# Optimization experiments

Measured on AMD Instinct MI355X. Metric: run time of the kernel, lower is better.

The kernel has to match this reference:

```python
import jax, jax.numpy as jnp
import numpy as np

MACRO_CURVE_ORDER = 3
MAX_ACTION_LEN = 24
NUM_CURVES = 8
VOCAB = 361
NUM_LAYERS = 6
HID = 32


def setup_inputs() -> dict:
    key = jax.random.key(0)
    ks = iter(jax.random.split(key, 32))
    B, N_PART, P, CTX = 4096, 100, 64, 64

    def lin(k, din, dout):
        k1, k2 = jax.random.split(k)
        s = 1.0 / np.sqrt(din)
        return (jax.random.uniform(k1, (din, dout), jnp.float32, -s, s),
                jax.random.uniform(k2, (dout,), jnp.float32, -s, s))

    fc1_w, fc1_b = lin(next(ks), P, 256)
    fc2_w, fc2_b = lin(next(ks), 256, 256)
    fc3_w, fc3_b = lin(next(ks), CTX + 256, 512)
    fc4_w, fc4_b = lin(next(ks), 512, 256)
    fc5_w, fc5_b = lin(next(ks), 256, 128)
    fc6_w, fc6_b = lin(next(ks), 128, 32)
    fc10_w, fc10_b = lin(next(ks), HID, VOCAB)

    s = 1.0 / np.sqrt(HID)
    lstm_wih = jax.random.uniform(next(ks), (NUM_LAYERS, HID, 4 * HID), jnp.float32, -s, s)
    lstm_whh = jax.random.uniform(next(ks), (NUM_LAYERS, HID, 4 * HID), jnp.float32, -s, s)
    lstm_bih = jax.random.uniform(next(ks), (NUM_LAYERS, 4 * HID), jnp.float32, -s, s)
    lstm_bhh = jax.random.uniform(next(ks), (NUM_LAYERS, 4 * HID), jnp.float32, -s, s)

    return {
        "c": jax.random.normal(next(ks), (B, CTX), jnp.float32),
        "x": jax.random.normal(next(ks), (B, N_PART * P), jnp.float32),
        "hidden": jnp.zeros((NUM_LAYERS, B, HID), jnp.float32),
        "cell": jnp.zeros((NUM_LAYERS, B, HID), jnp.float32),
        "fc1_w": fc1_w, "fc1_b": fc1_b, "fc2_w": fc2_w, "fc2_b": fc2_b,
        "fc3_w": fc3_w, "fc3_b": fc3_b, "fc4_w": fc4_w, "fc4_b": fc4_b,
        "fc5_w": fc5_w, "fc5_b": fc5_b, "fc6_w": fc6_w, "fc6_b": fc6_b,
        "lstm_wih": lstm_wih, "lstm_whh": lstm_whh,
        "lstm_bih": lstm_bih, "lstm_bhh": lstm_bhh,
        "fc10_w": fc10_w, "fc10_b": fc10_b,
        "particle_size": P,
    }


def _lstm_stack(x, h, c, wih, whh, bih, bhh):
    """One time step through 6 stacked LSTM layers (PyTorch cell math)."""
    hs, cs = [], []
    inp = x
    for l in range(NUM_LAYERS):
        gates = inp @ wih[l] + bih[l] + h[l] @ whh[l] + bhh[l]  # (B, 4*HID)
        i, f, g, o = jnp.split(gates, 4, axis=-1)
        i, f, o = jax.nn.sigmoid(i), jax.nn.sigmoid(f), jax.nn.sigmoid(o)
        g = jnp.tanh(g)
        c_new = f * c[l] + i * g
        h_new = o * jnp.tanh(c_new)
        hs.append(h_new)
        cs.append(c_new)
        inp = h_new
    return inp, jnp.stack(hs), jnp.stack(cs)


def reference(c, x, hidden, cell, fc1_w, fc1_b, fc2_w, fc2_b, fc3_w, fc3_b,
              fc4_w, fc4_b, fc5_w, fc5_b, fc6_w, fc6_b,
              lstm_wih, lstm_whh, lstm_bih, lstm_bhh, fc10_w, fc10_b,
              particle_size):
    B = x.shape[0]
    # Belief (particle) encoder with mean pooling.
    xp = x.reshape(B, -1, particle_size)
    xp = jax.nn.relu(xp @ fc1_w + fc1_b)
    xp = jax.nn.relu(xp @ fc2_w + fc2_b)
    xp = xp.mean(axis=-2)  # (B, 256)
    z = jnp.concatenate([c, xp], axis=-1)
    z = jax.nn.relu(z @ fc3_w + fc3_b)
    z = jax.nn.relu(z @ fc4_w + fc4_b)
    z = jax.nn.relu(z @ fc5_w + fc5_b)
    z = jax.nn.relu(z @ fc6_w + fc6_b)  # (B, 32)

    def step(carry, _):
        xt, h, cst = carry
        xt, h, cst = _lstm_stack(xt, h, cst, lstm_wih, lstm_whh, lstm_bih, lstm_bhh)
        logits = xt @ fc10_w + fc10_b  # (B, VOCAB)
        idx = jax.lax.top_k(logits, NUM_CURVES)[1]  # (B, NUM_CURVES)
        return (xt, h, cst), idx

    (_, _, _), idxs = jax.lax.scan(step, (z, hidden, cell), None, length=MAX_ACTION_LEN)
    # (T, B, K) -> (B, T*K)
    preds = jnp.transpose(idxs, (1, 0, 2)).reshape(B, MAX_ACTION_LEN * NUM_CURVES)
    return preds
```

## Files before the change

kernel.cpp:

```cpp
#include <hip/hip_runtime.h>
#include <math.h>

#define BATCH 4096
#define NPART 100
#define PSZ   64

__device__ __forceinline__ void fma4(float4& d, const float s, const float4 v) {
    d.x = fmaf(s, v.x, d.x); d.y = fmaf(s, v.y, d.y);
    d.z = fmaf(s, v.z, d.z); d.w = fmaf(s, v.w, d.w);
}
__device__ __forceinline__ float4 addrelu4(const float4 a, const float4 b) {
    return make_float4(fmaxf(a.x + b.x, 0.f), fmaxf(a.y + b.y, 0.f),
                       fmaxf(a.z + b.z, 0.f), fmaxf(a.w + b.w, 0.f));
}

typedef const __attribute__((address_space(1))) unsigned int  gu32;
typedef __attribute__((address_space(3)))       unsigned int  lu32;
__device__ __forceinline__ void gload_lds16(const float* g, float* l) {
    __builtin_amdgcn_global_load_lds((gu32*)g, (lu32*)l, 16, 0, 0);
}

__device__ __forceinline__ void stage_panel16(const float* __restrict__ w,
                                              float* dst, const int p,
                                              const int wv, const int lane) {
    const float* g = w + p * 4096 + wv * 256 + lane * 4;
    float*       l = dst + wv * 256;
    #pragma unroll
    for (int s = 0; s < 4; ++s)
        gload_lds16(g + s * 1024, l + s * 1024);
}

template<int NRR>
__device__ __forceinline__ void enc_chunk(
    const float* __restrict__ xb, const int rbase,
    const float* __restrict__ w1c, const float* __restrict__ w2,
    float* __restrict__ h1s, float* __restrict__ wpan,
    const int wv, const int lane, const int rg, const int col0,
    const float4 b1a, const float4 b1b, const float4 b2a, const float4 b2b,
    float* msum)
{
    stage_panel16(w2, wpan, 0, wv, lane);

    int rowr[NRR];
    #pragma unroll
    for (int rr = 0; rr < NRR; ++rr)
        rowr[rr] = rbase + ((NRR == 1 && rg >= 4) ? 0 : (rg + 8 * rr));

    float4 a0[NRR], a1[NRR];
    #pragma unroll
    for (int rr = 0; rr < NRR; ++rr) {
        a0[rr] = make_float4(0.f, 0.f, 0.f, 0.f);
        a1[rr] = make_float4(0.f, 0.f, 0.f, 0.f);
    }
    #pragma unroll 2
    for (int k0 = 0; k0 < 64; k0 += 4) {
        float4 bva[4], bvb[4];
        #pragma unroll
        for (int kk = 0; kk < 4; ++kk) {
            bva[kk] = *(const float4*)(w1c + (k0 + kk) * 256);
            bvb[kk] = *(const float4*)(w1c + (k0 + kk) * 256 + 4);
        }
        #pragma unroll
        for (int rr = 0; rr < NRR; ++rr) {
            const float4 av = *(const float4*)(xb + (size_t)rowr[rr] * 64 + k0);
            fma4(a0[rr], av.x, bva[0]); fma4(a0[rr], av.y, bva[1]);
            fma4(a0[rr], av.z, bva[2]); fma4(a0[rr], av.w, bva[3]);
            fma4(a1[rr], av.x, bvb[0]); fma4(a1[rr], av.y, bvb[1]);
            fma4(a1[rr], av.z, bvb[2]); fma4(a1[rr], av.w, bvb[3]);
        }
    }
    #pragma unroll
    for (int rr = 0; rr < NRR; ++rr) {
        const int r = rg + 8 * rr;
        *(float4*)&h1s[r * 260 + col0]     = addrelu4(a0[rr], b1a);
        *(float4*)&h1s[r * 260 + col0 + 4] = addrelu4(a1[rr], b1b);
    }
    __syncthreads();

    float4 c0[NRR], c1[NRR];
    #pragma unroll
    for (int rr = 0; rr < NRR; ++rr) {
        c0[rr] = make_float4(0.f, 0.f, 0.f, 0.f);
        c1[rr] = make_float4(0.f, 0.f, 0.f, 0.f);
    }
    #pragma unroll 1
    for (int p = 0; p < 16; ++p) {
        if (p < 15)
            stage_panel16(w2, wpan + ((p + 1) & 1) * 4096, p + 1, wv, lane);
        const float* wp = wpan + (p & 1) * 4096;
        #pragma unroll
        for (int it = 0; it < 4; ++it) {
            const int kk0 = it * 4;
            float4 bva[4], bvb[4];
            #pragma unroll
            for (int kk = 0; kk < 4; ++kk) {
                bva[kk] = *(const float4*)&wp[(kk0 + kk) * 256 + col0];
                bvb[kk] = *(const float4*)&wp[(kk0 + kk) * 256 + col0 + 4];
            }
            const int kg = p * 16 + kk0;
            #pragma unroll
            for (int rr = 0; rr < NRR; ++rr) {
                const float4 av = *(const float4*)&h1s[(rg + 8 * rr) * 260 + kg];
                fma4(c0[rr], av.x, bva[0]); fma4(c0[rr], av.y, bva[1]);
                fma4(c0[rr], av.z, bva[2]); fma4(c0[rr], av.w, bva[3]);
                fma4(c1[rr], av.x, bvb[0]); fma4(c1[rr], av.y, bvb[1]);
                fma4(c1[rr], av.z, bvb[2]); fma4(c1[rr], av.w, bvb[3]);
            }
        }
        __syncthreads();
    }

    #pragma unroll
    for (int rr = 0; rr < NRR; ++rr) {
        if (NRR == 4 || rg < 4) {
            msum[0] += fmaxf(c0[rr].x + b2a.x, 0.f);
            msum[1] += fmaxf(c0[rr].y + b2a.y, 0.f);
            msum[2] += fmaxf(c0[rr].z + b2a.z, 0.f);
            msum[3] += fmaxf(c0[rr].w + b2a.w, 0.f);
            msum[4] += fmaxf(c1[rr].x + b2b.x, 0.f);
            msum[5] += fmaxf(c1[rr].y + b2b.y, 0.f);
            msum[6] += fmaxf(c1[rr].z + b2b.z, 0.f);
            msum[7] += fmaxf(c1[rr].w + b2b.w, 0.f);
        }
    }
}

__global__ __launch_bounds__(256) void k_encoder(
    const float* __restrict__ x,
    const float* __restrict__ w1, const float* __restrict__ b1,
    const float* __restrict__ w2, const float* __restrict__ b2,
    float* __restrict__ xp)
{
    __shared__ __align__(16) float h1s[32 * 260];
    __shared__ __align__(16) float wpan[2 * 16 * 256];
    const int tid  = threadIdx.x;
    const int b    = blockIdx.x;
    const int lane = tid & 63;
    const int wv   = tid >> 6;
    const int cgw  = lane & 7;
    const int rg   = lane >> 3;
    const int col0 = wv * 64 + cgw * 8;

    const float* xb  = x + (size_t)b * (NPART * PSZ);
    const float* w1c = w1 + col0;
    const float4 b1a = *(const float4*)&b1[col0];
    const float4 b1b = *(const float4*)&b1[col0 + 4];
    const float4 b2a = *(const float4*)&b2[col0];
    const float4 b2b = *(const float4*)&b2[col0 + 4];

    float msum[8] = {0.f,0.f,0.f,0.f,0.f,0.f,0.f,0.f};

    enc_chunk<4>(xb,  0, w1c, w2, h1s, wpan, wv, lane, rg, col0, b1a, b1b, b2a, b2b, msum);
    enc_chunk<4>(xb, 32, w1c, w2, h1s, wpan, wv, lane, rg, col0, b1a, b1b, b2a, b2b, msum);
    enc_chunk<4>(xb, 64, w1c, w2, h1s, wpan, wv, lane, rg, col0, b1a, b1b, b2a, b2b, msum);
    enc_chunk<1>(xb, 96, w1c, w2, h1s, wpan, wv, lane, rg, col0, b1a, b1b, b2a, b2b, msum);

    #pragma unroll
    for (int q = 0; q < 8; ++q) {
        msum[q] += __shfl_xor(msum[q], 8, 64);
        msum[q] += __shfl_xor(msum[q], 16, 64);
        msum[q] += __shfl_xor(msum[q], 32, 64);
    }
    if (rg == 0) {
        float4 o0 = make_float4(msum[0] / 100.f, msum[1] / 100.f,
                                msum[2] / 100.f, msum[3] / 100.f);
        float4 o1 = make_float4(msum[4] / 100.f, msum[5] / 100.f,
                                msum[6] / 100.f, msum[7] / 100.f);
        *(float4*)&xp[(size_t)b * 256 + col0]     = o0;
        *(float4*)&xp[(size_t)b * 256 + col0 + 4] = o1;
    }
}

__global__ __launch_bounds__(256) void k_mlpstm(
    const float* __restrict__ cin, const float* __restrict__ xp,
    const float* __restrict__ w3, const float* __restrict__ b3,
    const float* __restrict__ w4, const float* __restrict__ b4,
    const float* __restrict__ w5, const float* __restrict__ b5,
    const float* __restrict__ w6, const float* __restrict__ b6,
    const float* __restrict__ hid0, const float* __restrict__ cel0,
    const float* __restrict__ wih, const float* __restrict__ whh,
    const float* __restrict__ bih, const float* __restrict__ bhh,
    const float* __restrict__ w10, const float* __restrict__ b10,
    int* __restrict__ out)
{
    __shared__ __align__(16) float smem[15432];
    float (*in0)[320]    = (float(*)[320])(smem);
    float (*h3)[512]     = (float(*)[512])(smem + 2560);
    float (*h4)[256]     = (float(*)[256])(smem + 6656);
    float (*h5)[128]     = (float(*)[128])(smem + 8704);
    float (*xs)[32]      = (float(*)[32])(smem);
    float (*hs)[8][32]   = (float(*)[8][32])(smem + 256);
    float (*cs)[8][32]   = (float(*)[8][32])(smem + 1792);
    float (*gates)[128]  = (float(*)[128])(smem + 3328);
    float (*logits)[361] = (float(*)[361])(smem + 4352);
    float* wldsI         = smem + 7240;
    float* wldsH         = smem + 11336;

    const int tid  = threadIdx.x;
    const int row0 = blockIdx.x * 8;
    const int lane = tid & 63, wv = tid >> 6;

    for (int i = tid; i < 8 * 16; i += 256) {
        int r = i >> 4, q = i & 15;
        *(float4*)&in0[r][q * 4] = *(const float4*)&cin[(size_t)(row0 + r) * 64 + q * 4];
    }
    for (int i = tid; i < 8 * 64; i += 256) {
        int r = i >> 6, q = i & 63;
        *(float4*)&in0[r][64 + q * 4] = *(const float4*)&xp[(size_t)(row0 + r) * 256 + q * 4];
    }
    __syncthreads();

    {
        float a0[8], a1[8];
        #pragma unroll
        for (int r = 0; r < 8; ++r) { a0[r] = 0.f; a1[r] = 0.f; }
        const int c0 = tid, c1 = tid + 256;
        for (int kq = 0; kq < 80; ++kq) {
            const int k0 = kq * 4;
            float wa0 = w3[(k0+0)*512 + c0], wa1 = w3[(k0+1)*512 + c0];
            float wa2 = w3[(k0+2)*512 + c0], wa3 = w3[(k0+3)*512 + c0];
            float wb0 = w3[(k0+0)*512 + c1], wb1 = w3[(k0+1)*512 + c1];
            float wb2 = w3[(k0+2)*512 + c1], wb3 = w3[(k0+3)*512 + c1];
            #pragma unroll
            for (int r = 0; r < 8; ++r) {
                const float4 a = *(const float4*)&in0[r][k0];
                a0[r] = fmaf(a.x, wa0, fmaf(a.y, wa1, fmaf(a.z, wa2, fmaf(a.w, wa3, a0[r]))));
                a1[r] = fmaf(a.x, wb0, fmaf(a.y, wb1, fmaf(a.z, wb2, fmaf(a.w, wb3, a1[r]))));
            }
        }
        const float bb0 = b3[c0], bb1 = b3[c1];
        #pragma unroll
        for (int r = 0; r < 8; ++r) {
            h3[r][c0] = fmaxf(a0[r] + bb0, 0.f);
            h3[r][c1] = fmaxf(a1[r] + bb1, 0.f);
        }
    }
    __syncthreads();

    {
        float ac[8];
        #pragma unroll
        for (int r = 0; r < 8; ++r) ac[r] = 0.f;
        for (int kq = 0; kq < 128; ++kq) {
            const int k0 = kq * 4;
            float w0 = w4[(k0+0)*256 + tid], w1v = w4[(k0+1)*256 + tid];
            float w2v = w4[(k0+2)*256 + tid], w3v = w4[(k0+3)*256 + tid];
            #pragma unroll
            for (int r = 0; r < 8; ++r) {
                const float4 a = *(const float4*)&h3[r][k0];
                ac[r] = fmaf(a.x, w0, fmaf(a.y, w1v, fmaf(a.z, w2v, fmaf(a.w, w3v, ac[r]))));
            }
        }
        const float bb = b4[tid];
        #pragma unroll
        for (int r = 0; r < 8; ++r) h4[r][tid] = fmaxf(ac[r] + bb, 0.f);
    }
    __syncthreads();

    {
        const int c5 = tid & 127, half = tid >> 7;
        float ac[4];
        #pragma unroll
        for (int r = 0; r < 4; ++r) ac[r] = 0.f;
        for (int kq = 0; kq < 64; ++kq) {
            const int k0 = kq * 4;
            float w0 = w5[(k0+0)*128 + c5], w1v = w5[(k0+1)*128 + c5];
            float w2v = w5[(k0+2)*128 + c5], w3v = w5[(k0+3)*128 + c5];
            #pragma unroll
            for (int r = 0; r < 4; ++r) {
                const float4 a = *(const float4*)&h4[half * 4 + r][k0];
                ac[r] = fmaf(a.x, w0, fmaf(a.y, w1v, fmaf(a.z, w2v, fmaf(a.w, w3v, ac[r]))));
            }
        }
        const float bb = b5[c5];
        #pragma unroll
        for (int r = 0; r < 4; ++r) h5[half * 4 + r][c5] = fmaxf(ac[r] + bb, 0.f);
    }
    __syncthreads();

    {
        const int c6 = tid & 31, r = tid >> 5;
        float ac = 0.f;
        for (int kq = 0; kq < 32; ++kq) {
            const int k0 = kq * 4;
            float w0 = w6[(k0+0)*32 + c6], w1v = w6[(k0+1)*32 + c6];
            float w2v = w6[(k0+2)*32 + c6], w3v = w6[(k0+3)*32 + c6];
            const float4 a = *(const float4*)&h5[r][k0];
            ac = fmaf(a.x, w0, fmaf(a.y, w1v, fmaf(a.z, w2v, fmaf(a.w, w3v, ac))));
        }
        xs[r][c6] = fmaxf(ac + b6[c6], 0.f);
    }
    __syncthreads();

    stage_panel16(wih, wldsI, 0, wv, lane);
    stage_panel16(whh, wldsH, 0, wv, lane);

    for (int i = tid; i < 6 * 8 * 32; i += 256) {
        int l = i >> 8, rj = i & 255;
        (&hs[0][0][0])[i] = hid0[(size_t)l * BATCH * 32 + (size_t)row0 * 32 + rj];
        (&cs[0][0][0])[i] = cel0[(size_t)l * BATCH * 32 + (size_t)row0 * 32 + rj];
    }
    __syncthreads();

    const int g  = tid & 127, rg = tid >> 7;
    const int jc = tid & 31,  jr = tid >> 5;

    for (int t = 0; t < 24; ++t) {
        for (int l = 0; l < 6; ++l) {
            const float* inp = (l == 0) ? ((t == 0) ? &xs[0][0] : &hs[5][0][0])
                                        : &hs[l - 1][0][0];
            const float bsum = bih[l * 128 + g] + bhh[l * 128 + g];
            float acc[4] = {bsum, bsum, bsum, bsum};
            #pragma unroll
            for (int k = 0; k < 32; k += 4) {
                float wi0 = wldsI[(k+0)*128 + g], wi1 = wldsI[(k+1)*128 + g];
                float wi2 = wldsI[(k+2)*128 + g], wi3 = wldsI[(k+3)*128 + g];
                float wh0 = wldsH[(k+0)*128 + g], wh1 = wldsH[(k+1)*128 + g];
                float wh2 = wldsH[(k+2)*128 + g], wh3 = wldsH[(k+3)*128 + g];
                #pragma unroll
                for (int rr = 0; rr < 4; ++rr) {
                    const int r = rg * 4 + rr;
                    const float4 ai = *(const float4*)&inp[r * 32 + k];
                    const float4 ah = *(const float4*)&hs[l][r][k];
                    acc[rr] = fmaf(ai.x, wi0, acc[rr]); acc[rr] = fmaf(ai.y, wi1, acc[rr]);
                    acc[rr] = fmaf(ai.z, wi2, acc[rr]); acc[rr] = fmaf(ai.w, wi3, acc[rr]);
                    acc[rr] = fmaf(ah.x, wh0, acc[rr]); acc[rr] = fmaf(ah.y, wh1, acc[rr]);
                    acc[rr] = fmaf(ah.z, wh2, acc[rr]); acc[rr] = fmaf(ah.w, wh3, acc[rr]);
                }
            }
            #pragma unroll
            for (int rr = 0; rr < 4; ++rr) gates[rg * 4 + rr][g] = acc[rr];
            __syncthreads();

            {
                const int ln = (l + 1) % 6;
                stage_panel16(wih, wldsI, ln, wv, lane);
                stage_panel16(whh, wldsH, ln, wv, lane);
            }

            {
                const float gi = gates[jr][jc],      gf = gates[jr][32 + jc];
                const float gg = gates[jr][64 + jc], go = gates[jr][96 + jc];
                const float i_ = 1.f / (1.f + expf(-gi));
                const float f_ = 1.f / (1.f + expf(-gf));
                const float o_ = 1.f / (1.f + expf(-go));
                const float g_ = tanhf(gg);
                const float cn = f_ * cs[l][jr][jc] + i_ * g_;
                cs[l][jr][jc] = cn;
                hs[l][jr][jc] = o_ * tanhf(cn);
            }
            __syncthreads();
        }

        #pragma unroll
        for (int pass = 0; pass < 2; ++pass) {
            const int v = tid + pass * 256;
            if (v < 361) {
                const float bb = b10[v];
                float a8[8];
                #pragma unroll
                for (int r = 0; r < 8; ++r) a8[r] = bb;
                #pragma unroll
                for (int k = 0; k < 32; k += 4) {
                    float w0 = w10[(k+0)*361 + v], w1v = w10[(k+1)*361 + v];
                    float w2v = w10[(k+2)*361 + v], w3v = w10[(k+3)*361 + v];
                    #pragma unroll
                    for (int r = 0; r < 8; ++r) {
                        const float4 a = *(const float4*)&hs[5][r][k];
                        a8[r] = fmaf(a.x, w0, fmaf(a.y, w1v, fmaf(a.z, w2v, fmaf(a.w, w3v, a8[r]))));
                    }
                }
                #pragma unroll
                for (int r = 0; r < 8; ++r) logits[r][v] = a8[r];
            }
        }
        __syncthreads();

        for (int rr = 0; rr < 2; ++rr) {
            const int r = wv * 2 + rr;
            float val[6];
            #pragma unroll
            for (int s = 0; s < 6; ++s) {
                const int v = lane + 64 * s;
                val[s] = (v < 361) ? logits[r][v] : -3.4e38f;
            }
            unsigned msk = 0x3Fu;
            const int rowg = row0 + r;
            for (int sel = 0; sel < 8; ++sel) {
                float bv = -3.4e38f; int bi = 0x7FFFFFFF;
                #pragma unroll
                for (int s = 0; s < 6; ++s) {
                    if (msk & (1u << s)) {
                        const float v2 = val[s]; const int i2 = lane + 64 * s;
                        if (v2 > bv || (v2 == bv && i2 < bi)) { bv = v2; bi = i2; }
                    }
                }
                #pragma unroll
                for (int off = 32; off >= 1; off >>= 1) {
                    const float ov = __shfl_xor(bv, off, 64);
                    const int   oi = __shfl_xor(bi, off, 64);
                    if (ov > bv || (ov == bv && oi < bi)) { bv = ov; bi = oi; }
                }
                if ((bi & 63) == lane) msk &= ~(1u << (bi >> 6));
                if (lane == 0) out[(size_t)rowg * 192 + t * 8 + sel] = bi;
            }
        }
        __syncthreads();
    }
}

extern "C" void kernel_launch(void* const* d_in, const int* in_sizes, int n_in,
                              void* d_out, int out_size, void* d_ws, size_t ws_size,
                              hipStream_t stream) {
    const float* cin  = (const float*)d_in[0];
    const float* x    = (const float*)d_in[1];
    const float* hid0 = (const float*)d_in[2];
    const float* cel0 = (const float*)d_in[3];
    const float* w1 = (const float*)d_in[4];  const float* b1 = (const float*)d_in[5];
    const float* w2 = (const float*)d_in[6];  const float* b2 = (const float*)d_in[7];
    const float* w3 = (const float*)d_in[8];  const float* b3 = (const float*)d_in[9];
    const float* w4 = (const float*)d_in[10]; const float* b4 = (const float*)d_in[11];
    const float* w5 = (const float*)d_in[12]; const float* b5 = (const float*)d_in[13];
    const float* w6 = (const float*)d_in[14]; const float* b6 = (const float*)d_in[15];
    const float* wih = (const float*)d_in[16]; const float* whh = (const float*)d_in[17];
    const float* bih = (const float*)d_in[18]; const float* bhh = (const float*)d_in[19];
    const float* w10 = (const float*)d_in[20]; const float* b10 = (const float*)d_in[21];

    float* xp  = (float*)d_ws;
    int*   out = (int*)d_out;

    k_encoder<<<BATCH, 256, 0, stream>>>(x, w1, b1, w2, b2, xp);
    k_mlpstm<<<BATCH / 8, 256, 0, stream>>>(cin, xp, w3, b3, w4, b4, w5, b5, w6, b6,
                                            hid0, cel0, wih, whh, bih, bhh, w10, b10, out);
}
```

Measured before the change: 2.141 ms.

## Fuse fc10 logits into per-wave top-k registers with transposed fc10 weights

A small pre-kernel transposes fc10_w so each vocab entry's 32 weights are contiguous. In the LSTM kernel, each wave now computes logits only for the two rows it later ranks, keeping them in registers instead of writing them to a shared-memory logits buffer. This drops two block-wide barriers per time step and shrinks shared memory. The cost is less weight reuse: each weight is now read by four waves, and there is an extra kernel launch.

```diff
diff --git a/kernel.cpp b/kernel.cpp
--- a/kernel.cpp
+++ b/kernel.cpp
@@ -28,6 +28,16 @@
     #pragma unroll
     for (int s = 0; s < 4; ++s)
         gload_lds16(g + s * 1024, l + s * 1024);
+}
+
+__global__ __launch_bounds__(256) void k_tw10(
+    const float* __restrict__ w10, float* __restrict__ w10t)
+{
+    const int i = blockIdx.x * 256 + threadIdx.x;
+    if (i < 361 * 32) {
+        const int v = i >> 5, k = i & 31;
+        w10t[i] = w10[k * 361 + v];
+    }
 }
 
 template<int NRR>
@@ -180,21 +190,20 @@
     const float* __restrict__ hid0, const float* __restrict__ cel0,
     const float* __restrict__ wih, const float* __restrict__ whh,
     const float* __restrict__ bih, const float* __restrict__ bhh,
-    const float* __restrict__ w10, const float* __restrict__ b10,
+    const float* __restrict__ w10t, const float* __restrict__ b10,
     int* __restrict__ out)
 {
-    __shared__ __align__(16) float smem[15432];
-    float (*in0)[320]    = (float(*)[320])(smem);
-    float (*h3)[512]     = (float(*)[512])(smem + 2560);
-    float (*h4)[256]     = (float(*)[256])(smem + 6656);
-    float (*h5)[128]     = (float(*)[128])(smem + 8704);
-    float (*xs)[32]      = (float(*)[32])(smem);
-    float (*hs)[8][32]   = (float(*)[8][32])(smem + 256);
-    float (*cs)[8][32]   = (float(*)[8][32])(smem + 1792);
-    float (*gates)[128]  = (float(*)[128])(smem + 3328);
-    float (*logits)[361] = (float(*)[361])(smem + 4352);
-    float* wldsI         = smem + 7240;
-    float* wldsH         = smem + 11336;
+    __shared__ __align__(16) float smem[12544];
+    float (*in0)[320]   = (float(*)[320])(smem);
+    float (*h3)[512]    = (float(*)[512])(smem + 2560);
+    float (*h4)[256]    = (float(*)[256])(smem + 6656);
+    float (*h5)[128]    = (float(*)[128])(smem + 8704);
+    float (*xs)[32]     = (float(*)[32])(smem);
+    float (*hs)[8][32]  = (float(*)[8][32])(smem + 256);
+    float (*cs)[8][32]  = (float(*)[8][32])(smem + 1792);
+    float (*gates)[128] = (float(*)[128])(smem + 3328);
+    float* wldsI        = smem + 4352;
+    float* wldsH        = smem + 8448;
 
     const int tid  = threadIdx.x;
     const int row0 = blockIdx.x * 8;
@@ -304,6 +313,7 @@
 
     const int g  = tid & 127, rg = tid >> 7;
     const int jc = tid & 31,  jr = tid >> 5;
+    const int r0 = wv * 2, r1 = r0 + 1;
 
     for (int t = 0; t < 24; ++t) {
         for (int l = 0; l < 6; ++l) {
@@ -352,40 +362,33 @@
             __syncthreads();
         }
 
-        #pragma unroll
-        for (int pass = 0; pass < 2; ++pass) {
-            const int v = tid + pass * 256;
+        float val0[6], val1[6];
+        #pragma unroll
+        for (int s = 0; s < 6; ++s) {
+            const int v = lane + 64 * s;
             if (v < 361) {
                 const float bb = b10[v];
-                float a8[8];
-                #pragma unroll
-                for (int r = 0; r < 8; ++r) a8[r] = bb;
+                const float* wv4 = w10t + v * 32;
+                float p0 = bb, p1 = bb;
                 #pragma unroll
                 for (int k = 0; k < 32; k += 4) {
-                    float w0 = w10[(k+0)*361 + v], w1v = w10[(k+1)*361 + v];
-                    float w2v = w10[(k+2)*361 + v], w3v = w10[(k+3)*361 + v];
-                    #pragma unroll
-                    for (int r = 0; r < 8; ++r) {
-                        const float4 a = *(const float4*)&hs[5][r][k];
-                        a8[r] = fmaf(a.x, w0, fmaf(a.y, w1v, fmaf(a.z, w2v, fmaf(a.w, w3v, a8[r]))));
-                    }
+                    const float4 w4v = *(const float4*)&wv4[k];
+                    const float4 a0 = *(const float4*)&hs[5][r0][k];
+                    const float4 a1 = *(const float4*)&hs[5][r1][k];
+                    p0 = fmaf(a0.x, w4v.x, fmaf(a0.y, w4v.y, fmaf(a0.z, w4v.z, fmaf(a0.w, w4v.w, p0))));
+                    p1 = fmaf(a1.x, w4v.x, fmaf(a1.y, w4v.y, fmaf(a1.z, w4v.z, fmaf(a1.w, w4v.w, p1))));
                 }
-                #pragma unroll
-                for (int r = 0; r < 8; ++r) logits[r][v] = a8[r];
-            }
-        }
-        __syncthreads();
-
+                val0[s] = p0; val1[s] = p1;
+            } else {
+                val0[s] = -3.4e38f; val1[s] = -3.4e38f;
+            }
+        }
+
+        #pragma unroll 1
         for (int rr = 0; rr < 2; ++rr) {
-            const int r = wv * 2 + rr;
-            float val[6];
-            #pragma unroll
-            for (int s = 0; s < 6; ++s) {
-                const int v = lane + 64 * s;
-                val[s] = (v < 361) ? logits[r][v] : -3.4e38f;
-            }
+            const float* val = (rr == 0) ? val0 : val1;
+            const int rowg = row0 + r0 + rr;
             unsigned msk = 0x3Fu;
-            const int rowg = row0 + r;
             for (int sel = 0; sel < 8; ++sel) {
                 float bv = -3.4e38f; int bi = 0x7FFFFFFF;
                 #pragma unroll
@@ -405,7 +408,6 @@
                 if (lane == 0) out[(size_t)rowg * 192 + t * 8 + sel] = bi;
             }
         }
-        __syncthreads();
     }
 }
 
@@ -426,10 +428,12 @@
     const float* bih = (const float*)d_in[18]; const float* bhh = (const float*)d_in[19];
     const float* w10 = (const float*)d_in[20]; const float* b10 = (const float*)d_in[21];
 
-    float* xp  = (float*)d_ws;
-    int*   out = (int*)d_out;
-
+    float* xp   = (float*)d_ws;
+    float* w10t = xp + (size_t)BATCH * 256;
+    int*   out  = (int*)d_out;
+
+    k_tw10<<<46, 256, 0, stream>>>(w10, w10t);
     k_encoder<<<BATCH, 256, 0, stream>>>(x, w1, b1, w2, b2, xp);
     k_mlpstm<<<BATCH / 8, 256, 0, stream>>>(cin, xp, w3, b3, w4, b4, w5, b5, w6, b6,
-                                            hid0, cel0, wih, whh, bih, bhh, w10, b10, out);
-}
+                                            hid0, cel0, wih, whh, bih, bhh, w10t, b10, out);
+}
```

After: 2.721 ms. +27.1%, slower.
